# Kernel tuning notes

Hardware: AMD Instinct MI355X
Metric: run time of the kernel (lower is better)

## Reference

```python
import jax, jax.numpy as jnp
import numpy as np

B, N, IN_F, OUT_F, H, NUM_EDGE_TYPES = 16, 512, 256, 256, 8, 50
HEAD_DIM = OUT_F // H
LN_EPS = 1e-5


def setup_inputs() -> dict:
    key = jax.random.key(0)
    ks = jax.random.split(key, 8)
    x = jax.random.normal(ks[0], (B, N, IN_F), dtype=jnp.float32)
    adj = jax.random.randint(ks[1], (B, N, N), 0, 2, dtype=jnp.int32)
    edge_types = jax.random.randint(ks[2], (B, N, N), 0, NUM_EDGE_TYPES, dtype=jnp.int32)
    # Parameters (torch Linear stores weight as [out, in]; we keep [in, out] for x @ W)
    W = jax.random.normal(ks[3], (IN_F, OUT_F), dtype=jnp.float32) / np.sqrt(IN_F)
    a1 = jax.random.normal(ks[4], (HEAD_DIM,), dtype=jnp.float32) / np.sqrt(HEAD_DIM)
    a2 = jax.random.normal(ks[5], (HEAD_DIM,), dtype=jnp.float32) / np.sqrt(HEAD_DIM)
    edge_emb = jax.random.normal(ks[6], (NUM_EDGE_TYPES, H), dtype=jnp.float32) * 0.02
    edge_emb = edge_emb.at[0].set(0.0)  # padding_idx=0
    ln_gamma = jnp.ones((OUT_F,), dtype=jnp.float32)
    ln_beta = jnp.zeros((OUT_F,), dtype=jnp.float32)
    return {"x": x, "adj": adj, "edge_types": edge_types, "W": W, "a1": a1,
            "a2": a2, "edge_emb": edge_emb, "ln_gamma": ln_gamma, "ln_beta": ln_beta}


def reference(x, adj, edge_types, W, a1, a2, edge_emb, ln_gamma, ln_beta):
    Bx, Nx, _ = x.shape
    # Wh: [B, N, H, D]
    Wh = (x @ W).reshape(Bx, Nx, H, HEAD_DIM)
    # per-node attention scalars: [B, N, H]
    s1 = jnp.einsum('bnhd,d->bnh', Wh, a1)
    s2 = jnp.einsum('bnhd,d->bnh', Wh, a2)
    # e: [B, N(i), N(j), H]
    e = s1[:, :, None, :] + s2[:, None, :, :] + edge_emb[edge_types]
    e = jnp.where(e > 0, e, 0.2 * e)  # leaky_relu(0.2)
    e = jnp.where((adj == 0)[..., None], jnp.float32(-1e9), e)
    alpha = jax.nn.softmax(e, axis=2)  # softmax over j
    # (dropout omitted: eval mode / deterministic reference)
    h = jnp.einsum('bijh,bjhd->bihd', alpha, Wh).reshape(Bx, Nx, OUT_F)
    # LayerNorm over last dim
    mu = jnp.mean(h, axis=-1, keepdims=True)
    var = jnp.mean(jnp.square(h - mu), axis=-1, keepdims=True)
    hn = (h - mu) * jax.lax.rsqrt(var + LN_EPS) * ln_gamma + ln_beta
    return jax.nn.elu(hn)
```

## Files before the change

kernel.cpp:

```cpp
#include <hip/hip_runtime.h>
#include <hip/hip_bf16.h>
#include <stdint.h>

namespace gat {
constexpr int NB   = 16;
constexpr int NN   = 512;
constexpr int FIN  = 256;
constexpr int FOUT = 256;
constexpr int H    = 8;
constexpr int NE   = 50;
constexpr float L2E  = 1.4426950408889634f;
constexpr float MASK = -115.41500f;
}
using namespace gat;

typedef __attribute__((ext_vector_type(8))) short short8;
typedef __attribute__((ext_vector_type(4))) float f32x4;

__device__ __forceinline__ unsigned pk_bf16(unsigned ulo, unsigned uhi) {
  return __builtin_amdgcn_perm(uhi, ulo, 0x07060302u);
}
__device__ __forceinline__ unsigned pk2f(float a, float b) {
  return pk_bf16(__float_as_uint(a) + 0x8000u, __float_as_uint(b) + 0x8000u);
}
__device__ __forceinline__ unsigned short bf1(float a) {
  return (unsigned short)((__float_as_uint(a) + 0x8000u) >> 16);
}

__global__ __launch_bounds__(256) void k_pre(const int* __restrict__ adj,
                                             const int* __restrict__ ety,
                                             const float* __restrict__ Wm,
                                             const float* __restrict__ a1,
                                             const float* __restrict__ a2,
                                             unsigned* __restrict__ codes,
                                             unsigned short* __restrict__ WbTa) {
  const int blk = blockIdx.x;
  if (blk < 1024) {
    const size_t base = ((size_t)blk * 256 + threadIdx.x) * 16;
    const int4* ap = (const int4*)(adj + base);
    const int4* ep = (const int4*)(ety + base);
    unsigned o[4];
    #pragma unroll
    for (int g = 0; g < 4; ++g) {
      const int4 a = ap[g];
      const int4 e = ep[g];
      o[g] = (unsigned)(e.x | (a.x << 6))
           | ((unsigned)(e.y | (a.y << 6)) << 8)
           | ((unsigned)(e.z | (a.z << 6)) << 16)
           | ((unsigned)(e.w | (a.w << 6)) << 24);
    }
    uint4 v; v.x = o[0]; v.y = o[1]; v.z = o[2]; v.w = o[3];
    *(uint4*)(codes + base / 4) = v;
  } else if (blk < 1280) {
    const int k = blk - 1024;
    const int f = threadIdx.x;
    WbTa[f * FIN + k] = bf1(Wm[k * FOUT + f]);
  } else {
    const int k = threadIdx.x;
    const float* wr = Wm + (size_t)k * FOUT;
    #pragma unroll
    for (int h = 0; h < H; ++h) {
      float v1 = 0.f, v2 = 0.f;
      #pragma unroll
      for (int d = 0; d < 32; ++d) {
        const float wv = wr[h * 32 + d];
        v1 += wv * a1[d];
        v2 += wv * a2[d];
      }
      WbTa[(256 + h) * FIN + k] = bf1(v1);
      WbTa[(264 + h) * FIN + k] = bf1(v2);
    }
  }
}

__global__ __launch_bounds__(256, 4) void k_gemm(
    const float* __restrict__ x, const unsigned short* __restrict__ WbTa,
    unsigned short* __restrict__ WhT, float* __restrict__ s1T, float* __restrict__ s2T)
{
  __shared__ alignas(16) unsigned short xS[16 * 264];
  const int t    = threadIdx.x;
  const int row0 = blockIdx.x * 16;

  {
    const int r  = t >> 4;
    const int kb = (t & 15) * 16;
    const float4* xg = (const float4*)(x + (size_t)(row0 + r) * FIN + kb);
    const float4 v0 = xg[0], v1 = xg[1], v2 = xg[2], v3 = xg[3];
    uint4 o0, o1;
    o0.x = pk2f(v0.x, v0.y); o0.y = pk2f(v0.z, v0.w);
    o0.z = pk2f(v1.x, v1.y); o0.w = pk2f(v1.z, v1.w);
    o1.x = pk2f(v2.x, v2.y); o1.y = pk2f(v2.z, v2.w);
    o1.z = pk2f(v3.x, v3.y); o1.w = pk2f(v3.z, v3.w);
    *(uint4*)&xS[r * 264 + kb]     = o0;
    *(uint4*)&xS[r * 264 + kb + 8] = o1;
  }
  __syncthreads();

  const int w    = t >> 6;
  const int L    = t & 63;
  const int nn   = L & 15;
  const int quad = L >> 4;
  const unsigned short* wb = WbTa + (size_t)(w * 64 + nn) * FIN + quad * 8;
  const unsigned short* wa = WbTa + (size_t)(256 + nn) * FIN + quad * 8;
  const unsigned short* xp = &xS[nn * 264 + quad * 8];

  f32x4 acc0 = {0.f,0.f,0.f,0.f}, acc1 = {0.f,0.f,0.f,0.f};
  f32x4 acc2 = {0.f,0.f,0.f,0.f}, acc3 = {0.f,0.f,0.f,0.f};
  f32x4 accA = {0.f,0.f,0.f,0.f};

  #pragma unroll
  for (int kc = 0; kc < 8; ++kc) {
    const int k0 = kc * 32;
    const short8 A  = *(const short8*)(xp + k0);
    const short8 B0 = *(const short8*)(wb + k0);
    const short8 B1 = *(const short8*)(wb + 16 * FIN + k0);
    const short8 B2 = *(const short8*)(wb + 32 * FIN + k0);
    const short8 B3 = *(const short8*)(wb + 48 * FIN + k0);
    acc0 = __builtin_amdgcn_mfma_f32_16x16x32_bf16(A, B0, acc0, 0, 0, 0);
    acc1 = __builtin_amdgcn_mfma_f32_16x16x32_bf16(A, B1, acc1, 0, 0, 0);
    acc2 = __builtin_amdgcn_mfma_f32_16x16x32_bf16(A, B2, acc2, 0, 0, 0);
    acc3 = __builtin_amdgcn_mfma_f32_16x16x32_bf16(A, B3, acc3, 0, 0, 0);
    if (w == 3) {
      const short8 BA = *(const short8*)(wa + k0);
      accA = __builtin_amdgcn_mfma_f32_16x16x32_bf16(A, BA, accA, 0, 0, 0);
    }
  }

  const int b     = row0 >> 9;
  const int node0 = (row0 & 511) + quad * 4;
  f32x4 accs[4] = {acc0, acc1, acc2, acc3};

  #pragma unroll
  for (int ft = 0; ft < 4; ++ft) {
    const int f = w * 64 + ft * 16 + nn;
    uint2 o;
    o.x = pk2f(accs[ft][0], accs[ft][1]);
    o.y = pk2f(accs[ft][2], accs[ft][3]);
    *(uint2*)(WhT + (size_t)((b * 8 + (f >> 5)) * 32 + (f & 31)) * 512 + node0) = o;
  }

  if (w == 3) {
    float4 sv;
    sv.x = accA[0] * L2E; sv.y = accA[1] * L2E;
    sv.z = accA[2] * L2E; sv.w = accA[3] * L2E;
    float* dst = (nn < 8) ? (s1T + (size_t)(b * 8 + nn) * 512 + node0)
                          : (s2T + (size_t)(b * 8 + (nn - 8)) * 512 + node0);
    *(float4*)dst = sv;
  }
}

__global__ __launch_bounds__(512, 4) void k_attn(
    const unsigned char* __restrict__ codes,
    const float* __restrict__ s1T, const float* __restrict__ s2T,
    const unsigned short* __restrict__ WhT, const float* __restrict__ emb,
    const float* __restrict__ gam, const float* __restrict__ bet,
    float* __restrict__ out)
{
  __shared__ float2 embS[4 * 64];
  __shared__ float2 lnS[16 * 4];
  __shared__ float  s2S[8 * 512];
  __shared__ float  redS[256 * 18];

  const int t    = threadIdx.x;
  const int b    = blockIdx.x >> 5;
  const int i0   = (blockIdx.x & 31) * 16;
  const int W    = t >> 6;
  const int w    = W & 3;
  const int jh   = W >> 2;
  const int L    = t & 63;
  const int i    = L & 15;
  const int quad = L >> 4;
  const int h0   = w, h1 = w + 4;

  {
    const float4* sg = (const float4*)(s2T + (size_t)b * 8 * 512);
    float4* ss = (float4*)s2S;
    ss[t]       = sg[t];
    ss[t + 512] = sg[t + 512];
  }
  if (t < 256) {
    const int wp = t >> 6, e = t & 63;
    if (e < NE) {
      float2 v; v.x = emb[e * H + wp] * L2E; v.y = emb[e * H + wp + 4] * L2E;
      embS[t] = v;
    }
  }

  const int row   = b * NN + i0 + i;
  const int jbase = jh * 256;

  uint2 cw[8];
  {
    const unsigned char* cp = codes + (size_t)row * NN + jbase + quad * 8;
    #pragma unroll
    for (int kc = 0; kc < 8; ++kc) cw[kc] = *(const uint2*)(cp + kc * 32);
  }

  const float si0 = s1T[(size_t)(b * 8 + h0) * 512 + i0 + i];
  const float si1 = s1T[(size_t)(b * 8 + h1) * 512 + i0 + i];
  const unsigned short* wt00 = WhT + (size_t)((b * 8 + h0) * 32 + i)      * 512;
  const unsigned short* wt01 = WhT + (size_t)((b * 8 + h0) * 32 + 16 + i) * 512;
  const unsigned short* wt10 = WhT + (size_t)((b * 8 + h1) * 32 + i)      * 512;
  const unsigned short* wt11 = WhT + (size_t)((b * 8 + h1) * 32 + 16 + i) * 512;

  f32x4 acc00 = {0.f,0.f,0.f,0.f}, acc01 = {0.f,0.f,0.f,0.f};
  f32x4 acc10 = {0.f,0.f,0.f,0.f}, acc11 = {0.f,0.f,0.f,0.f};
  float l0 = 0.f, l1 = 0.f;

  const int ja0 = jbase + quad * 8;
  short8 nA00 = *(const short8*)(wt00 + ja0);
  short8 nA01 = *(const short8*)(wt01 + ja0);
  short8 nA10 = *(const short8*)(wt10 + ja0);
  short8 nA11 = *(const short8*)(wt11 + ja0);

  __syncthreads();

  #pragma unroll
  for (int kc = 0; kc < 8; ++kc) {
    const int ja  = jbase + kc * 32 + quad * 8;
    const short8 A00 = nA00, A01 = nA01, A10 = nA10, A11 = nA11;
    {
      const int jn = ja + 32;
      nA00 = *(const short8*)(wt00 + jn);
      nA01 = *(const short8*)(wt01 + jn);
      nA10 = *(const short8*)(wt10 + jn);
      nA11 = *(const short8*)(wt11 + jn);
    }
    const float4 sa0 = *(const float4*)&s2S[h0 * 512 + ja];
    const float4 sb0 = *(const float4*)&s2S[h0 * 512 + ja + 4];
    const float4 sa1 = *(const float4*)&s2S[h1 * 512 + ja];
    const float4 sb1 = *(const float4*)&s2S[h1 * 512 + ja + 4];

    const float s20[8] = {sa0.x, sa0.y, sa0.z, sa0.w, sb0.x, sb0.y, sb0.z, sb0.w};
    const float s21[8] = {sa1.x, sa1.y, sa1.z, sa1.w, sb1.x, sb1.y, sb1.z, sb1.w};

    unsigned u0[8], u1[8];
    #pragma unroll
    for (int q = 0; q < 8; ++q) {
      const unsigned cword = (q < 4) ? cw[kc].x : cw[kc].y;
      const unsigned c = (cword >> ((q & 3) * 8)) & 0x7fu;
      const bool on = c >= 64u;
      const float2 em = embS[w * 64 + (c & 63u)];
      float e0 = si0 + s20[q] + em.x;
      float e1 = si1 + s21[q] + em.y;
      e0 = fmaxf(e0, 0.2f * e0);
      e1 = fmaxf(e1, 0.2f * e1);
      e0 = on ? e0 : MASK;
      e1 = on ? e1 : MASK;
      const float p0 = exp2f(e0);
      const float p1 = exp2f(e1);
      l0 += p0; l1 += p1;
      u0[q] = __float_as_uint(p0) + 0x8000u;
      u1[q] = __float_as_uint(p1) + 0x8000u;
    }
    uint4 U0, U1;
    U0.x = pk_bf16(u0[0], u0[1]); U0.y = pk_bf16(u0[2], u0[3]);
    U0.z = pk_bf16(u0[4], u0[5]); U0.w = pk_bf16(u0[6], u0[7]);
    U1.x = pk_bf16(u1[0], u1[1]); U1.y = pk_bf16(u1[2], u1[3]);
    U1.z = pk_bf16(u1[4], u1[5]); U1.w = pk_bf16(u1[6], u1[7]);
    const short8 B0 = __builtin_bit_cast(short8, U0);
    const short8 B1 = __builtin_bit_cast(short8, U1);

    acc00 = __builtin_amdgcn_mfma_f32_16x16x32_bf16(A00, B0, acc00, 0, 0, 0);
    acc01 = __builtin_amdgcn_mfma_f32_16x16x32_bf16(A01, B0, acc01, 0, 0, 0);
    acc10 = __builtin_amdgcn_mfma_f32_16x16x32_bf16(A10, B1, acc10, 0, 0, 0);
    acc11 = __builtin_amdgcn_mfma_f32_16x16x32_bf16(A11, B1, acc11, 0, 0, 0);
  }

  l0 += __shfl_xor(l0, 16); l0 += __shfl_xor(l0, 32);
  l1 += __shfl_xor(l1, 16); l1 += __shfl_xor(l1, 32);

  const int tt = (w << 6) | L;
  if (jh == 1) {
    float* rp = redS + tt * 18;
    rp[0]=acc00[0]; rp[1]=acc00[1]; rp[2]=acc00[2]; rp[3]=acc00[3];
    rp[4]=acc01[0]; rp[5]=acc01[1]; rp[6]=acc01[2]; rp[7]=acc01[3];
    rp[8]=acc10[0]; rp[9]=acc10[1]; rp[10]=acc10[2]; rp[11]=acc10[3];
    rp[12]=acc11[0]; rp[13]=acc11[1]; rp[14]=acc11[2]; rp[15]=acc11[3];
    rp[16]=l0; rp[17]=l1;
  }
  __syncthreads();

  float vals[16]; float mu, rstd;
  if (jh == 0) {
    const float* rp = redS + tt * 18;
    acc00[0]+=rp[0]; acc00[1]+=rp[1]; acc00[2]+=rp[2]; acc00[3]+=rp[3];
    acc01[0]+=rp[4]; acc01[1]+=rp[5]; acc01[2]+=rp[6]; acc01[3]+=rp[7];
    acc10[0]+=rp[8]; acc10[1]+=rp[9]; acc10[2]+=rp[10]; acc10[3]+=rp[11];
    acc11[0]+=rp[12]; acc11[1]+=rp[13]; acc11[2]+=rp[14]; acc11[3]+=rp[15];
    l0 += rp[16]; l1 += rp[17];
    const float inv0 = __builtin_amdgcn_rcpf(l0);
    const float inv1 = __builtin_amdgcn_rcpf(l1);
    #pragma unroll
    for (int r = 0; r < 4; ++r) {
      vals[r]      = acc00[r] * inv0;
      vals[4 + r]  = acc01[r] * inv0;
      vals[8 + r]  = acc10[r] * inv1;
      vals[12 + r] = acc11[r] * inv1;
    }
    float s = 0.f, ss = 0.f;
    #pragma unroll
    for (int k = 0; k < 16; ++k) { s += vals[k]; ss += vals[k] * vals[k]; }
    s += __shfl_xor(s, 16); ss += __shfl_xor(ss, 16);
    s += __shfl_xor(s, 32); ss += __shfl_xor(ss, 32);
    if (quad == 0) { float2 v; v.x = s; v.y = ss; lnS[i * 4 + w] = v; }
  }
  __syncthreads();
  if (jh == 1) return;

  {
    float S = 0.f, SS = 0.f;
    #pragma unroll
    for (int ww = 0; ww < 4; ++ww) { const float2 v = lnS[i * 4 + ww]; S += v.x; SS += v.y; }
    mu = S * (1.0f / 256.0f);
    const float var = SS * (1.0f / 256.0f) - mu * mu;
    rstd = rsqrtf(var + 1e-5f);
  }

  const int fb[4] = { h0 * 32 + quad * 4, h0 * 32 + 16 + quad * 4,
                      h1 * 32 + quad * 4, h1 * 32 + 16 + quad * 4 };
  #pragma unroll
  for (int g = 0; g < 4; ++g) {
    const float4 gv = *(const float4*)(gam + fb[g]);
    const float4 bv = *(const float4*)(bet + fb[g]);
    float4 o;
    o.x = (vals[g*4+0] - mu) * rstd * gv.x + bv.x;
    o.y = (vals[g*4+1] - mu) * rstd * gv.y + bv.y;
    o.z = (vals[g*4+2] - mu) * rstd * gv.z + bv.z;
    o.w = (vals[g*4+3] - mu) * rstd * gv.w + bv.w;
    o.x = o.x > 0.f ? o.x : exp2f(o.x * L2E) - 1.f;
    o.y = o.y > 0.f ? o.y : exp2f(o.y * L2E) - 1.f;
    o.z = o.z > 0.f ? o.z : exp2f(o.z * L2E) - 1.f;
    o.w = o.w > 0.f ? o.w : exp2f(o.w * L2E) - 1.f;
    *(float4*)(out + (size_t)row * FOUT + fb[g]) = o;
  }
}

extern "C" void kernel_launch(void* const* d_in, const int* in_sizes, int n_in,
                              void* d_out, int out_size, void* d_ws, size_t ws_size,
                              hipStream_t stream) {
  (void)in_sizes; (void)n_in; (void)out_size; (void)ws_size;
  const float* x   = (const float*)d_in[0];
  const int*   adj = (const int*)  d_in[1];
  const int*   ety = (const int*)  d_in[2];
  const float* Wm  = (const float*)d_in[3];
  const float* a1  = (const float*)d_in[4];
  const float* a2  = (const float*)d_in[5];
  const float* emb = (const float*)d_in[6];
  const float* gam = (const float*)d_in[7];
  const float* bet = (const float*)d_in[8];
  float* out = (float*)d_out;

  unsigned short* WhT  = (unsigned short*)d_ws;
  unsigned short* WbTa = WhT + (size_t)NB * H * 32 * 512;
  float* s1T  = (float*)(WbTa + (size_t)272 * FIN);
  float* s2T  = s1T + (size_t)NB * H * NN;
  unsigned char* codes = (unsigned char*)(s2T + (size_t)NB * H * NN);

  k_pre<<<dim3(1281), dim3(256), 0, stream>>>(adj, ety, Wm, a1, a2, (unsigned*)codes, WbTa);
  k_gemm<<<dim3(NB * NN / 16), dim3(256), 0, stream>>>(x, WbTa, WhT, s1T, s2T);
  k_attn<<<dim3(NB * (NN / 16)), dim3(512), 0, stream>>>(codes, s1T, s2T, WhT, emb, gam, bet, out);
}
```

Measured before the change: 136.8 us.

## Fuse pre, GEMM and attention kernels into one cooperative kernel with grid syncs

Merges the three kernel launches into a single cooperative kernel of 512 blocks of 512 threads. Two grid-wide barriers separate the packing, projection and attention phases. The GEMM phase is reshaped so eight waves each cover 32 output features. The goal is to remove launch gaps and inter-kernel drain time. In exchange it pays for grid-sync overhead, fixes occupancy for every phase at one shape, and needs all 512 blocks co-resident; the old three-kernel path remains as a fallback if the cooperative launch fails.

Measured after the change: 266.8 us. 1.95x slower.

```diff
diff --git a/kernel.cpp b/kernel.cpp
--- a/kernel.cpp
+++ b/kernel.cpp
@@ -1,6 +1,9 @@
 #include <hip/hip_runtime.h>
 #include <hip/hip_bf16.h>
+#include <hip/hip_cooperative_groups.h>
 #include <stdint.h>
+
+namespace cg = cooperative_groups;
 
 namespace gat {
 constexpr int NB   = 16;
@@ -27,16 +30,28 @@
   return (unsigned short)((__float_as_uint(a) + 0x8000u) >> 16);
 }
 
-__global__ __launch_bounds__(256) void k_pre(const int* __restrict__ adj,
-                                             const int* __restrict__ ety,
-                                             const float* __restrict__ Wm,
-                                             const float* __restrict__ a1,
-                                             const float* __restrict__ a2,
-                                             unsigned* __restrict__ codes,
-                                             unsigned short* __restrict__ WbTa) {
+__global__ __launch_bounds__(512, 4) void k_fused(
+    const int* __restrict__ adj, const int* __restrict__ ety,
+    const float* __restrict__ x, const float* __restrict__ Wm,
+    const float* __restrict__ a1, const float* __restrict__ a2,
+    const float* __restrict__ emb, const float* __restrict__ gam,
+    const float* __restrict__ bet, float* __restrict__ out,
+    unsigned short* __restrict__ WhT, unsigned short* __restrict__ WbTa,
+    float* __restrict__ s1T, float* __restrict__ s2T,
+    unsigned char* __restrict__ codes)
+{
+  __shared__ __align__(16) char smem[37376];
+  float2* embS = (float2*)smem;
+  float2* lnS  = (float2*)(smem + 2048);
+  float*  s2S  = (float*)(smem + 2560);
+  float*  redS = (float*)(smem + 18944);
+  unsigned short* xS = (unsigned short*)smem;
+
   const int blk = blockIdx.x;
-  if (blk < 1024) {
-    const size_t base = ((size_t)blk * 256 + threadIdx.x) * 16;
+  const int t   = threadIdx.x;
+
+  {
+    const size_t base = ((size_t)blk * 512 + t) * 16;
     const int4* ap = (const int4*)(adj + base);
     const int4* ep = (const int4*)(ety + base);
     unsigned o[4];
@@ -50,126 +65,94 @@
            | ((unsigned)(e.w | (a.w << 6)) << 24);
     }
     uint4 v; v.x = o[0]; v.y = o[1]; v.z = o[2]; v.w = o[3];
-    *(uint4*)(codes + base / 4) = v;
-  } else if (blk < 1280) {
-    const int k = blk - 1024;
-    const int f = threadIdx.x;
-    WbTa[f * FIN + k] = bf1(Wm[k * FOUT + f]);
-  } else {
-    const int k = threadIdx.x;
-    const float* wr = Wm + (size_t)k * FOUT;
-    #pragma unroll
-    for (int h = 0; h < H; ++h) {
-      float v1 = 0.f, v2 = 0.f;
+    *(uint4*)(codes + base) = v;
+  }
+  if (blk < 256) {
+    if (t < 256) WbTa[t * FIN + blk] = bf1(Wm[blk * FOUT + t]);
+  } else if (blk == 256) {
+    if (t < 256) {
+      const int k = t;
+      const float* wr = Wm + (size_t)k * FOUT;
       #pragma unroll
-      for (int d = 0; d < 32; ++d) {
-        const float wv = wr[h * 32 + d];
-        v1 += wv * a1[d];
-        v2 += wv * a2[d];
+      for (int h = 0; h < H; ++h) {
+        float v1 = 0.f, v2 = 0.f;
+        #pragma unroll
+        for (int d = 0; d < 32; ++d) {
+          const float wv = wr[h * 32 + d];
+          v1 += wv * a1[d];
+          v2 += wv * a2[d];
+        }
+        WbTa[(256 + h) * FIN + k] = bf1(v1);
+        WbTa[(264 + h) * FIN + k] = bf1(v2);
       }
-      WbTa[(256 + h) * FIN + k] = bf1(v1);
-      WbTa[(264 + h) * FIN + k] = bf1(v2);
-    }
-  }
-}
-
-__global__ __launch_bounds__(256, 4) void k_gemm(
-    const float* __restrict__ x, const unsigned short* __restrict__ WbTa,
-    unsigned short* __restrict__ WhT, float* __restrict__ s1T, float* __restrict__ s2T)
-{
-  __shared__ alignas(16) unsigned short xS[16 * 264];
-  const int t    = threadIdx.x;
-  const int row0 = blockIdx.x * 16;
-
-  {
-    const int r  = t >> 4;
-    const int kb = (t & 15) * 16;
+    }
+  }
+  cg::this_grid().sync();
+
+  const int row0 = blk * 16;
+  {
+    const int r  = t >> 5;
+    const int kb = (t & 31) * 8;
     const float4* xg = (const float4*)(x + (size_t)(row0 + r) * FIN + kb);
-    const float4 v0 = xg[0], v1 = xg[1], v2 = xg[2], v3 = xg[3];
-    uint4 o0, o1;
-    o0.x = pk2f(v0.x, v0.y); o0.y = pk2f(v0.z, v0.w);
-    o0.z = pk2f(v1.x, v1.y); o0.w = pk2f(v1.z, v1.w);
-    o1.x = pk2f(v2.x, v2.y); o1.y = pk2f(v2.z, v2.w);
-    o1.z = pk2f(v3.x, v3.y); o1.w = pk2f(v3.z, v3.w);
-    *(uint4*)&xS[r * 264 + kb]     = o0;
-    *(uint4*)&xS[r * 264 + kb + 8] = o1;
-  }
-  __syncthreads();
-
-  const int w    = t >> 6;
+    const float4 v0 = xg[0], v1 = xg[1];
+    uint4 o;
+    o.x = pk2f(v0.x, v0.y); o.y = pk2f(v0.z, v0.w);
+    o.z = pk2f(v1.x, v1.y); o.w = pk2f(v1.z, v1.w);
+    *(uint4*)&xS[r * 264 + kb] = o;
+  }
+  __syncthreads();
+
+  const int W8   = t >> 6;
   const int L    = t & 63;
   const int nn   = L & 15;
   const int quad = L >> 4;
-  const unsigned short* wb = WbTa + (size_t)(w * 64 + nn) * FIN + quad * 8;
-  const unsigned short* wa = WbTa + (size_t)(256 + nn) * FIN + quad * 8;
-  const unsigned short* xp = &xS[nn * 264 + quad * 8];
-
-  f32x4 acc0 = {0.f,0.f,0.f,0.f}, acc1 = {0.f,0.f,0.f,0.f};
-  f32x4 acc2 = {0.f,0.f,0.f,0.f}, acc3 = {0.f,0.f,0.f,0.f};
-  f32x4 accA = {0.f,0.f,0.f,0.f};
-
-  #pragma unroll
-  for (int kc = 0; kc < 8; ++kc) {
-    const int k0 = kc * 32;
-    const short8 A  = *(const short8*)(xp + k0);
-    const short8 B0 = *(const short8*)(wb + k0);
-    const short8 B1 = *(const short8*)(wb + 16 * FIN + k0);
-    const short8 B2 = *(const short8*)(wb + 32 * FIN + k0);
-    const short8 B3 = *(const short8*)(wb + 48 * FIN + k0);
-    acc0 = __builtin_amdgcn_mfma_f32_16x16x32_bf16(A, B0, acc0, 0, 0, 0);
-    acc1 = __builtin_amdgcn_mfma_f32_16x16x32_bf16(A, B1, acc1, 0, 0, 0);
-    acc2 = __builtin_amdgcn_mfma_f32_16x16x32_bf16(A, B2, acc2, 0, 0, 0);
-    acc3 = __builtin_amdgcn_mfma_f32_16x16x32_bf16(A, B3, acc3, 0, 0, 0);
-    if (w == 3) {
-      const short8 BA = *(const short8*)(wa + k0);
-      accA = __builtin_amdgcn_mfma_f32_16x16x32_bf16(A, BA, accA, 0, 0, 0);
-    }
-  }
-
-  const int b     = row0 >> 9;
-  const int node0 = (row0 & 511) + quad * 4;
-  f32x4 accs[4] = {acc0, acc1, acc2, acc3};
-
-  #pragma unroll
-  for (int ft = 0; ft < 4; ++ft) {
-    const int f = w * 64 + ft * 16 + nn;
-    uint2 o;
-    o.x = pk2f(accs[ft][0], accs[ft][1]);
-    o.y = pk2f(accs[ft][2], accs[ft][3]);
-    *(uint2*)(WhT + (size_t)((b * 8 + (f >> 5)) * 32 + (f & 31)) * 512 + node0) = o;
-  }
-
-  if (w == 3) {
-    float4 sv;
-    sv.x = accA[0] * L2E; sv.y = accA[1] * L2E;
-    sv.z = accA[2] * L2E; sv.w = accA[3] * L2E;
-    float* dst = (nn < 8) ? (s1T + (size_t)(b * 8 + nn) * 512 + node0)
-                          : (s2T + (size_t)(b * 8 + (nn - 8)) * 512 + node0);
-    *(float4*)dst = sv;
-  }
-}
-
-__global__ __launch_bounds__(512, 4) void k_attn(
-    const unsigned char* __restrict__ codes,
-    const float* __restrict__ s1T, const float* __restrict__ s2T,
-    const unsigned short* __restrict__ WhT, const float* __restrict__ emb,
-    const float* __restrict__ gam, const float* __restrict__ bet,
-    float* __restrict__ out)
-{
-  __shared__ float2 embS[4 * 64];
-  __shared__ float2 lnS[16 * 4];
-  __shared__ float  s2S[8 * 512];
-  __shared__ float  redS[256 * 18];
-
-  const int t    = threadIdx.x;
-  const int b    = blockIdx.x >> 5;
-  const int i0   = (blockIdx.x & 31) * 16;
-  const int W    = t >> 6;
-  const int w    = W & 3;
-  const int jh   = W >> 2;
-  const int L    = t & 63;
-  const int i    = L & 15;
-  const int quad = L >> 4;
+  {
+    const unsigned short* wb = WbTa + (size_t)(W8 * 32 + nn) * FIN + quad * 8;
+    const unsigned short* wa = WbTa + (size_t)(256 + nn) * FIN + quad * 8;
+    const unsigned short* xp = &xS[nn * 264 + quad * 8];
+
+    f32x4 acc0 = {0.f,0.f,0.f,0.f}, acc1 = {0.f,0.f,0.f,0.f}, accA = {0.f,0.f,0.f,0.f};
+    #pragma unroll
+    for (int kc = 0; kc < 8; ++kc) {
+      const int k0 = kc * 32;
+      const short8 A  = *(const short8*)(xp + k0);
+      const short8 B0 = *(const short8*)(wb + k0);
+      const short8 B1 = *(const short8*)(wb + 16 * FIN + k0);
+      acc0 = __builtin_amdgcn_mfma_f32_16x16x32_bf16(A, B0, acc0, 0, 0, 0);
+      acc1 = __builtin_amdgcn_mfma_f32_16x16x32_bf16(A, B1, acc1, 0, 0, 0);
+      if (W8 == 7) {
+        const short8 BA = *(const short8*)(wa + k0);
+        accA = __builtin_amdgcn_mfma_f32_16x16x32_bf16(A, BA, accA, 0, 0, 0);
+      }
+    }
+
+    const int b     = row0 >> 9;
+    const int node0 = (row0 & 511) + quad * 4;
+    f32x4 accs[2] = {acc0, acc1};
+    #pragma unroll
+    for (int ft = 0; ft < 2; ++ft) {
+      const int f = W8 * 32 + ft * 16 + nn;
+      uint2 o;
+      o.x = pk2f(accs[ft][0], accs[ft][1]);
+      o.y = pk2f(accs[ft][2], accs[ft][3]);
+      *(uint2*)(WhT + (size_t)((b * 8 + (f >> 5)) * 32 + (f & 31)) * 512 + node0) = o;
+    }
+    if (W8 == 7) {
+      float4 sv;
+      sv.x = accA[0] * L2E; sv.y = accA[1] * L2E;
+      sv.z = accA[2] * L2E; sv.w = accA[3] * L2E;
+      float* dst = (nn < 8) ? (s1T + (size_t)(b * 8 + nn) * 512 + node0)
+                            : (s2T + (size_t)(b * 8 + (nn - 8)) * 512 + node0);
+      *(float4*)dst = sv;
+    }
+  }
+  cg::this_grid().sync();
+
+  const int b    = blk >> 5;
+  const int i0   = (blk & 31) * 16;
+  const int w    = W8 & 3;
+  const int jh   = W8 >> 2;
+  const int i    = nn;
   const int h0   = w, h1 = w + 4;
 
   {
@@ -336,13 +319,312 @@
   }
 }
 
+__global__ __launch_bounds__(256) void k_pre(const int* __restrict__ adj,
+                                             const int* __restrict__ ety,
+                                             const float* __restrict__ Wm,
+                                             const float* __restrict__ a1,
+                                             const float* __restrict__ a2,
+                                             unsigned* __restrict__ codes,
+                                             unsigned short* __restrict__ WbTa) {
+  const int blk = blockIdx.x;
+  if (blk < 1024) {
+    const size_t base = ((size_t)blk * 256 + threadIdx.x) * 16;
+    const int4* ap = (const int4*)(adj + base);
+    const int4* ep = (const int4*)(ety + base);
+    unsigned o[4];
+    #pragma unroll
+    for (int g = 0; g < 4; ++g) {
+      const int4 a = ap[g];
+      const int4 e = ep[g];
+      o[g] = (unsigned)(e.x | (a.x << 6))
+           | ((unsigned)(e.y | (a.y << 6)) << 8)
+           | ((unsigned)(e.z | (a.z << 6)) << 16)
+           | ((unsigned)(e.w | (a.w << 6)) << 24);
+    }
+    uint4 v; v.x = o[0]; v.y = o[1]; v.z = o[2]; v.w = o[3];
+    *(uint4*)(codes + base / 4) = v;
+  } else if (blk < 1280) {
+    const int k = blk - 1024;
+    const int f = threadIdx.x;
+    WbTa[f * FIN + k] = bf1(Wm[k * FOUT + f]);
+  } else {
+    const int k = threadIdx.x;
+    const float* wr = Wm + (size_t)k * FOUT;
+    #pragma unroll
+    for (int h = 0; h < H; ++h) {
+      float v1 = 0.f, v2 = 0.f;
+      #pragma unroll
+      for (int d = 0; d < 32; ++d) {
+        const float wv = wr[h * 32 + d];
+        v1 += wv * a1[d];
+        v2 += wv * a2[d];
+      }
+      WbTa[(256 + h) * FIN + k] = bf1(v1);
+      WbTa[(264 + h) * FIN + k] = bf1(v2);
+    }
+  }
+}
+
+__global__ __launch_bounds__(256, 4) void k_gemm(
+    const float* __restrict__ x, const unsigned short* __restrict__ WbTa,
+    unsigned short* __restrict__ WhT, float* __restrict__ s1T, float* __restrict__ s2T)
+{
+  __shared__ alignas(16) unsigned short xS[16 * 264];
+  const int t    = threadIdx.x;
+  const int row0 = blockIdx.x * 16;
+  {
+    const int r  = t >> 4;
+    const int kb = (t & 15) * 16;
+    const float4* xg = (const float4*)(x + (size_t)(row0 + r) * FIN + kb);
+    const float4 v0 = xg[0], v1 = xg[1], v2 = xg[2], v3 = xg[3];
+    uint4 o0, o1;
+    o0.x = pk2f(v0.x, v0.y); o0.y = pk2f(v0.z, v0.w);
+    o0.z = pk2f(v1.x, v1.y); o0.w = pk2f(v1.z, v1.w);
+    o1.x = pk2f(v2.x, v2.y); o1.y = pk2f(v2.z, v2.w);
+    o1.z = pk2f(v3.x, v3.y); o1.w = pk2f(v3.z, v3.w);
+    *(uint4*)&xS[r * 264 + kb]     = o0;
+    *(uint4*)&xS[r * 264 + kb + 8] = o1;
+  }
+  __syncthreads();
+
+  const int w    = t >> 6;
+  const int L    = t & 63;
+  const int nn   = L & 15;
+  const int quad = L >> 4;
+  const unsigned short* wb = WbTa + (size_t)(w * 64 + nn) * FIN + quad * 8;
+  const unsigned short* wa = WbTa + (size_t)(256 + nn) * FIN + quad * 8;
+  const unsigned short* xp = &xS[nn * 264 + quad * 8];
+
+  f32x4 acc0 = {0.f,0.f,0.f,0.f}, acc1 = {0.f,0.f,0.f,0.f};
+  f32x4 acc2 = {0.f,0.f,0.f,0.f}, acc3 = {0.f,0.f,0.f,0.f};
+  f32x4 accA = {0.f,0.f,0.f,0.f};
+
+  #pragma unroll
+  for (int kc = 0; kc < 8; ++kc) {
+    const int k0 = kc * 32;
+    const short8 A  = *(const short8*)(xp + k0);
+    const short8 B0 = *(const short8*)(wb + k0);
+    const short8 B1 = *(const short8*)(wb + 16 * FIN + k0);
+    const short8 B2 = *(const short8*)(wb + 32 * FIN + k0);
+    const short8 B3 = *(const short8*)(wb + 48 * FIN + k0);
+    acc0 = __builtin_amdgcn_mfma_f32_16x16x32_bf16(A, B0, acc0, 0, 0, 0);
+    acc1 = __builtin_amdgcn_mfma_f32_16x16x32_bf16(A, B1, acc1, 0, 0, 0);
+    acc2 = __builtin_amdgcn_mfma_f32_16x16x32_bf16(A, B2, acc2, 0, 0, 0);
+    acc3 = __builtin_amdgcn_mfma_f32_16x16x32_bf16(A, B3, acc3, 0, 0, 0);
+    if (w == 3) {
+      const short8 BA = *(const short8*)(wa + k0);
+      accA = __builtin_amdgcn_mfma_f32_16x16x32_bf16(A, BA, accA, 0, 0, 0);
+    }
+  }
+
+  const int b     = row0 >> 9;
+  const int node0 = (row0 & 511) + quad * 4;
+  f32x4 accs[4] = {acc0, acc1, acc2, acc3};
+  #pragma unroll
+  for (int ft = 0; ft < 4; ++ft) {
+    const int f = w * 64 + ft * 16 + nn;
+    uint2 o;
+    o.x = pk2f(accs[ft][0], accs[ft][1]);
+    o.y = pk2f(accs[ft][2], accs[ft][3]);
+    *(uint2*)(WhT + (size_t)((b * 8 + (f >> 5)) * 32 + (f & 31)) * 512 + node0) = o;
+  }
+  if (w == 3) {
+    float4 sv;
+    sv.x = accA[0] * L2E; sv.y = accA[1] * L2E;
+    sv.z = accA[2] * L2E; sv.w = accA[3] * L2E;
+    float* dst = (nn < 8) ? (s1T + (size_t)(b * 8 + nn) * 512 + node0)
+                          : (s2T + (size_t)(b * 8 + (nn - 8)) * 512 + node0);
+    *(float4*)dst = sv;
+  }
+}
+
+__global__ __launch_bounds__(512, 4) void k_attn(
+    const unsigned char* __restrict__ codes,
+    const float* __restrict__ s1T, const float* __restrict__ s2T,
+    const unsigned short* __restrict__ WhT, const float* __restrict__ emb,
+    const float* __restrict__ gam, const float* __restrict__ bet,
+    float* __restrict__ out)
+{
+  __shared__ float2 embS[4 * 64];
+  __shared__ float2 lnS[16 * 4];
+  __shared__ float  s2S[8 * 512];
+  __shared__ float  redS[256 * 18];
+
+  const int t    = threadIdx.x;
+  const int b    = blockIdx.x >> 5;
+  const int i0   = (blockIdx.x & 31) * 16;
+  const int W    = t >> 6;
+  const int w    = W & 3;
+  const int jh   = W >> 2;
+  const int L    = t & 63;
+  const int i    = L & 15;
+  const int quad = L >> 4;
+  const int h0   = w, h1 = w + 4;
+
+  {
+    const float4* sg = (const float4*)(s2T + (size_t)b * 8 * 512);
+    float4* ss = (float4*)s2S;
+    ss[t]       = sg[t];
+    ss[t + 512] = sg[t + 512];
+  }
+  if (t < 256) {
+    const int wp = t >> 6, e = t & 63;
+    if (e < NE) {
+      float2 v; v.x = emb[e * H + wp] * L2E; v.y = emb[e * H + wp + 4] * L2E;
+      embS[t] = v;
+    }
+  }
+
+  const int row   = b * NN + i0 + i;
+  const int jbase = jh * 256;
+  uint2 cw[8];
+  {
+    const unsigned char* cp = codes + (size_t)row * NN + jbase + quad * 8;
+    #pragma unroll
+    for (int kc = 0; kc < 8; ++kc) cw[kc] = *(const uint2*)(cp + kc * 32);
+  }
+  const float si0 = s1T[(size_t)(b * 8 + h0) * 512 + i0 + i];
+  const float si1 = s1T[(size_t)(b * 8 + h1) * 512 + i0 + i];
+  const unsigned short* wt00 = WhT + (size_t)((b * 8 + h0) * 32 + i)      * 512;
+  const unsigned short* wt01 = WhT + (size_t)((b * 8 + h0) * 32 + 16 + i) * 512;
+  const unsigned short* wt10 = WhT + (size_t)((b * 8 + h1) * 32 + i)      * 512;
+  const unsigned short* wt11 = WhT + (size_t)((b * 8 + h1) * 32 + 16 + i) * 512;
+
+  f32x4 acc00 = {0.f,0.f,0.f,0.f}, acc01 = {0.f,0.f,0.f,0.f};
+  f32x4 acc10 = {0.f,0.f,0.f,0.f}, acc11 = {0.f,0.f,0.f,0.f};
+  float l0 = 0.f, l1 = 0.f;
+
+  const int ja0 = jbase + quad * 8;
+  short8 nA00 = *(const short8*)(wt00 + ja0);
+  short8 nA01 = *(const short8*)(wt01 + ja0);
+  short8 nA10 = *(const short8*)(wt10 + ja0);
+  short8 nA11 = *(const short8*)(wt11 + ja0);
+
+  __syncthreads();
+
+  #pragma unroll
+  for (int kc = 0; kc < 8; ++kc) {
+    const int ja  = jbase + kc * 32 + quad * 8;
+    const short8 A00 = nA00, A01 = nA01, A10 = nA10, A11 = nA11;
+    {
+      const int jn = ja + 32;
+      nA00 = *(const short8*)(wt00 + jn);
+      nA01 = *(const short8*)(wt01 + jn);
+      nA10 = *(const short8*)(wt10 + jn);
+      nA11 = *(const short8*)(wt11 + jn);
+    }
+    const float4 sa0 = *(const float4*)&s2S[h0 * 512 + ja];
+    const float4 sb0 = *(const float4*)&s2S[h0 * 512 + ja + 4];
+    const float4 sa1 = *(const float4*)&s2S[h1 * 512 + ja];
+    const float4 sb1 = *(const float4*)&s2S[h1 * 512 + ja + 4];
+    const float s20[8] = {sa0.x, sa0.y, sa0.z, sa0.w, sb0.x, sb0.y, sb0.z, sb0.w};
+    const float s21[8] = {sa1.x, sa1.y, sa1.z, sa1.w, sb1.x, sb1.y, sb1.z, sb1.w};
+    unsigned u0[8], u1[8];
+    #pragma unroll
+    for (int q = 0; q < 8; ++q) {
+      const unsigned cword = (q < 4) ? cw[kc].x : cw[kc].y;
+      const unsigned c = (cword >> ((q & 3) * 8)) & 0x7fu;
+      const bool on = c >= 64u;
+      const float2 em = embS[w * 64 + (c & 63u)];
+      float e0 = si0 + s20[q] + em.x;
+      float e1 = si1 + s21[q] + em.y;
+      e0 = fmaxf(e0, 0.2f * e0);
+      e1 = fmaxf(e1, 0.2f * e1);
+      e0 = on ? e0 : MASK;
+      e1 = on ? e1 : MASK;
+      const float p0 = exp2f(e0);
+      const float p1 = exp2f(e1);
+      l0 += p0; l1 += p1;
+      u0[q] = __float_as_uint(p0) + 0x8000u;
+      u1[q] = __float_as_uint(p1) + 0x8000u;
+    }
+    uint4 U0, U1;
+    U0.x = pk_bf16(u0[0], u0[1]); U0.y = pk_bf16(u0[2], u0[3]);
+    U0.z = pk_bf16(u0[4], u0[5]); U0.w = pk_bf16(u0[6], u0[7]);
+    U1.x = pk_bf16(u1[0], u1[1]); U1.y = pk_bf16(u1[2], u1[3]);
+    U1.z = pk_bf16(u1[4], u1[5]); U1.w = pk_bf16(u1[6], u1[7]);
+    const short8 B0 = __builtin_bit_cast(short8, U0);
+    const short8 B1 = __builtin_bit_cast(short8, U1);
+    acc00 = __builtin_amdgcn_mfma_f32_16x16x32_bf16(A00, B0, acc00, 0, 0, 0);
+    acc01 = __builtin_amdgcn_mfma_f32_16x16x32_bf16(A01, B0, acc01, 0, 0, 0);
+    acc10 = __builtin_amdgcn_mfma_f32_16x16x32_bf16(A10, B1, acc10, 0, 0, 0);
+    acc11 = __builtin_amdgcn_mfma_f32_16x16x32_bf16(A11, B1, acc11, 0, 0, 0);
+  }
+
+  l0 += __shfl_xor(l0, 16); l0 += __shfl_xor(l0, 32);
+  l1 += __shfl_xor(l1, 16); l1 += __shfl_xor(l1, 32);
+
+  const int tt = (w << 6) | L;
+  if (jh == 1) {
+    float* rp = redS + tt * 18;
+    rp[0]=acc00[0]; rp[1]=acc00[1]; rp[2]=acc00[2]; rp[3]=acc00[3];
+    rp[4]=acc01[0]; rp[5]=acc01[1]; rp[6]=acc01[2]; rp[7]=acc01[3];
+    rp[8]=acc10[0]; rp[9]=acc10[1]; rp[10]=acc10[2]; rp[11]=acc10[3];
+    rp[12]=acc11[0]; rp[13]=acc11[1]; rp[14]=acc11[2]; rp[15]=acc11[3];
+    rp[16]=l0; rp[17]=l1;
+  }
+  __syncthreads();
+
+  float vals[16]; float mu, rstd;
+  if (jh == 0) {
+    const float* rp = redS + tt * 18;
+    acc00[0]+=rp[0]; acc00[1]+=rp[1]; acc00[2]+=rp[2]; acc00[3]+=rp[3];
+    acc01[0]+=rp[4]; acc01[1]+=rp[5]; acc01[2]+=rp[6]; acc01[3]+=rp[7];
+    acc10[0]+=rp[8]; acc10[1]+=rp[9]; acc10[2]+=rp[10]; acc10[3]+=rp[11];
+    acc11[0]+=rp[12]; acc11[1]+=rp[13]; acc11[2]+=rp[14]; acc11[3]+=rp[15];
+    l0 += rp[16]; l1 += rp[17];
+    const float inv0 = __builtin_amdgcn_rcpf(l0);
+    const float inv1 = __builtin_amdgcn_rcpf(l1);
+    #pragma unroll
+    for (int r = 0; r < 4; ++r) {
+      vals[r]      = acc00[r] * inv0;
+      vals[4 + r]  = acc01[r] * inv0;
+      vals[8 + r]  = acc10[r] * inv1;
+      vals[12 + r] = acc11[r] * inv1;
+    }
+    float s = 0.f, ss = 0.f;
+    #pragma unroll
+    for (int k = 0; k < 16; ++k) { s += vals[k]; ss += vals[k] * vals[k]; }
+    s += __shfl_xor(s, 16); ss += __shfl_xor(ss, 16);
+    s += __shfl_xor(s, 32); ss += __shfl_xor(ss, 32);
+    if (quad == 0) { float2 v; v.x = s; v.y = ss; lnS[i * 4 + w] = v; }
+  }
+  __syncthreads();
+  if (jh == 1) return;
+  {
+    float S = 0.f, SS = 0.f;
+    #pragma unroll
+    for (int ww = 0; ww < 4; ++ww) { const float2 v = lnS[i * 4 + ww]; S += v.x; SS += v.y; }
+    mu = S * (1.0f / 256.0f);
+    const float var = SS * (1.0f / 256.0f) - mu * mu;
+    rstd = rsqrtf(var + 1e-5f);
+  }
+  const int fb[4] = { h0 * 32 + quad * 4, h0 * 32 + 16 + quad * 4,
+                      h1 * 32 + quad * 4, h1 * 32 + 16 + quad * 4 };
+  #pragma unroll
+  for (int g = 0; g < 4; ++g) {
+    const float4 gv = *(const float4*)(gam + fb[g]);
+    const float4 bv = *(const float4*)(bet + fb[g]);
+    float4 o;
+    o.x = (vals[g*4+0] - mu) * rstd * gv.x + bv.x;
+    o.y = (vals[g*4+1] - mu) * rstd * gv.y + bv.y;
+    o.z = (vals[g*4+2] - mu) * rstd * gv.z + bv.z;
+    o.w = (vals[g*4+3] - mu) * rstd * gv.w + bv.w;
+    o.x = o.x > 0.f ? o.x : exp2f(o.x * L2E) - 1.f;
+    o.y = o.y > 0.f ? o.y : exp2f(o.y * L2E) - 1.f;
+    o.z = o.z > 0.f ? o.z : exp2f(o.z * L2E) - 1.f;
+    o.w = o.w > 0.f ? o.w : exp2f(o.w * L2E) - 1.f;
+    *(float4*)(out + (size_t)row * FOUT + fb[g]) = o;
+  }
+}
+
 extern "C" void kernel_launch(void* const* d_in, const int* in_sizes, int n_in,
                               void* d_out, int out_size, void* d_ws, size_t ws_size,
                               hipStream_t stream) {
   (void)in_sizes; (void)n_in; (void)out_size; (void)ws_size;
-  const float* x   = (const float*)d_in[0];
   const int*   adj = (const int*)  d_in[1];
   const int*   ety = (const int*)  d_in[2];
+  const float* x   = (const float*)d_in[0];
   const float* Wm  = (const float*)d_in[3];
   const float* a1  = (const float*)d_in[4];
   const float* a2  = (const float*)d_in[5];
@@ -357,7 +639,14 @@
   float* s2T  = s1T + (size_t)NB * H * NN;
   unsigned char* codes = (unsigned char*)(s2T + (size_t)NB * H * NN);
 
-  k_pre<<<dim3(1281), dim3(256), 0, stream>>>(adj, ety, Wm, a1, a2, (unsigned*)codes, WbTa);
-  k_gemm<<<dim3(NB * NN / 16), dim3(256), 0, stream>>>(x, WbTa, WhT, s1T, s2T);
-  k_attn<<<dim3(NB * (NN / 16)), dim3(512), 0, stream>>>(codes, s1T, s2T, WhT, emb, gam, bet, out);
-}
+  void* args[] = { (void*)&adj, (void*)&ety, (void*)&x, (void*)&Wm, (void*)&a1,
+                   (void*)&a2, (void*)&emb, (void*)&gam, (void*)&bet, (void*)&out,
+                   (void*)&WhT, (void*)&WbTa, (void*)&s1T, (void*)&s2T, (void*)&codes };
+  hipError_t err = hipLaunchCooperativeKernel((const void*)k_fused, dim3(512), dim3(512),
+                                              args, 0, stream);
+  if (err != hipSuccess) {
+    k_pre<<<dim3(1281), dim3(256), 0, stream>>>(adj, ety, Wm, a1, a2, (unsigned*)codes, WbTa);
+    k_gemm<<<dim3(NB * NN / 16), dim3(256), 0, stream>>>(x, WbTa, WhT, s1T, s2T);
+    k_attn<<<dim3(NB * (NN / 16)), dim3(512), 0, stream>>>(codes, s1T, s2T, WhT, emb, gam, bet, out);
+  }
+}
```

## Fold mask into embedding table, compute softmax denominators via MFMA, merge pre-pass into GEMM

Applied to the files above, without the earlier changes.

Moves the adj/edge-type packing from the weight pre-pass into the GEMM launch as extra blocks, so the large packing work can run alongside the GEMM blocks in one launch. In the attention loop, the adjacency mask is folded into a 128-entry per-head embedding table, where masked entries hold a large negative bias, and this removes the per-element select. The row sums of exp are now taken by an extra MFMA against a ones vector, on the same bf16-truncated probabilities used for the weighted sum, which replaces the scalar accumulation and shuffles. Rounding is replaced by truncation plus a small bias added to the table entries, which changes numerics slightly.

Measured after the change: 138.4 us. About the same (+1.2%).

```diff
diff --git a/kernel.cpp b/kernel.cpp
--- a/kernel.cpp
+++ b/kernel.cpp
@@ -10,7 +10,8 @@
 constexpr int H    = 8;
 constexpr int NE   = 50;
 constexpr float L2E  = 1.4426950408889634f;
-constexpr float MASK = -115.41500f;
+constexpr float MASKB = -192.0f;
+constexpr float RBIAS = 0.00281502f;
 }
 using namespace gat;
 
@@ -27,32 +28,13 @@
   return (unsigned short)((__float_as_uint(a) + 0x8000u) >> 16);
 }
 
-__global__ __launch_bounds__(256) void k_pre(const int* __restrict__ adj,
-                                             const int* __restrict__ ety,
-                                             const float* __restrict__ Wm,
-                                             const float* __restrict__ a1,
-                                             const float* __restrict__ a2,
-                                             unsigned* __restrict__ codes,
-                                             unsigned short* __restrict__ WbTa) {
+__global__ __launch_bounds__(256) void k_prew(const float* __restrict__ Wm,
+                                              const float* __restrict__ a1,
+                                              const float* __restrict__ a2,
+                                              unsigned short* __restrict__ WbTa) {
   const int blk = blockIdx.x;
-  if (blk < 1024) {
-    const size_t base = ((size_t)blk * 256 + threadIdx.x) * 16;
-    const int4* ap = (const int4*)(adj + base);
-    const int4* ep = (const int4*)(ety + base);
-    unsigned o[4];
-    #pragma unroll
-    for (int g = 0; g < 4; ++g) {
-      const int4 a = ap[g];
-      const int4 e = ep[g];
-      o[g] = (unsigned)(e.x | (a.x << 6))
-           | ((unsigned)(e.y | (a.y << 6)) << 8)
-           | ((unsigned)(e.z | (a.z << 6)) << 16)
-           | ((unsigned)(e.w | (a.w << 6)) << 24);
-    }
-    uint4 v; v.x = o[0]; v.y = o[1]; v.z = o[2]; v.w = o[3];
-    *(uint4*)(codes + base / 4) = v;
-  } else if (blk < 1280) {
-    const int k = blk - 1024;
+  if (blk < 256) {
+    const int k = blk;
     const int f = threadIdx.x;
     WbTa[f * FIN + k] = bf1(Wm[k * FOUT + f]);
   } else {
@@ -73,14 +55,34 @@
   }
 }
 
-__global__ __launch_bounds__(256, 4) void k_gemm(
+__global__ __launch_bounds__(256, 4) void k_gp(
     const float* __restrict__ x, const unsigned short* __restrict__ WbTa,
-    unsigned short* __restrict__ WhT, float* __restrict__ s1T, float* __restrict__ s2T)
+    const int* __restrict__ adj, const int* __restrict__ ety,
+    unsigned short* __restrict__ WhT, float* __restrict__ s1T, float* __restrict__ s2T,
+    unsigned* __restrict__ codes)
 {
+  const int t = threadIdx.x;
+  if (blockIdx.x >= 512) {
+    const size_t base = ((size_t)(blockIdx.x - 512) * 256 + t) * 16;
+    const int4* ap = (const int4*)(adj + base);
+    const int4* ep = (const int4*)(ety + base);
+    unsigned o[4];
+    #pragma unroll
+    for (int g = 0; g < 4; ++g) {
+      const int4 a = ap[g];
+      const int4 e = ep[g];
+      o[g] = (unsigned)(e.x | (a.x << 6))
+           | ((unsigned)(e.y | (a.y << 6)) << 8)
+           | ((unsigned)(e.z | (a.z << 6)) << 16)
+           | ((unsigned)(e.w | (a.w << 6)) << 24);
+    }
+    uint4 v; v.x = o[0]; v.y = o[1]; v.z = o[2]; v.w = o[3];
+    *(uint4*)(codes + base / 4) = v;
+    return;
+  }
+
   __shared__ alignas(16) unsigned short xS[16 * 264];
-  const int t    = threadIdx.x;
   const int row0 = blockIdx.x * 16;
-
   {
     const int r  = t >> 4;
     const int kb = (t & 15) * 16;
@@ -129,7 +131,6 @@
   const int b     = row0 >> 9;
   const int node0 = (row0 & 511) + quad * 4;
   f32x4 accs[4] = {acc0, acc1, acc2, acc3};
-
   #pragma unroll
   for (int ft = 0; ft < 4; ++ft) {
     const int f = w * 64 + ft * 16 + nn;
@@ -138,7 +139,6 @@
     o.y = pk2f(accs[ft][2], accs[ft][3]);
     *(uint2*)(WhT + (size_t)((b * 8 + (f >> 5)) * 32 + (f & 31)) * 512 + node0) = o;
   }
-
   if (w == 3) {
     float4 sv;
     sv.x = accA[0] * L2E; sv.y = accA[1] * L2E;
@@ -156,7 +156,7 @@
     const float* __restrict__ gam, const float* __restrict__ bet,
     float* __restrict__ out)
 {
-  __shared__ float2 embS[4 * 64];
+  __shared__ float2 embS[4 * 128];
   __shared__ float2 lnS[16 * 4];
   __shared__ float  s2S[8 * 512];
   __shared__ float  redS[256 * 18];
@@ -178,24 +178,26 @@
     ss[t]       = sg[t];
     ss[t + 512] = sg[t + 512];
   }
-  if (t < 256) {
-    const int wp = t >> 6, e = t & 63;
-    if (e < NE) {
-      float2 v; v.x = emb[e * H + wp] * L2E; v.y = emb[e * H + wp + 4] * L2E;
-      embS[t] = v;
-    }
+  {
+    const int wp = t >> 7, c = t & 127;
+    float2 v;
+    if (c >= 64 && c < 64 + NE) {
+      v.x = emb[(c - 64) * H + wp]     * L2E + RBIAS;
+      v.y = emb[(c - 64) * H + wp + 4] * L2E + RBIAS;
+    } else {
+      v.x = MASKB; v.y = MASKB;
+    }
+    embS[t] = v;
   }
 
   const int row   = b * NN + i0 + i;
   const int jbase = jh * 256;
-
   uint2 cw[8];
   {
     const unsigned char* cp = codes + (size_t)row * NN + jbase + quad * 8;
     #pragma unroll
     for (int kc = 0; kc < 8; ++kc) cw[kc] = *(const uint2*)(cp + kc * 32);
   }
-
   const float si0 = s1T[(size_t)(b * 8 + h0) * 512 + i0 + i];
   const float si1 = s1T[(size_t)(b * 8 + h1) * 512 + i0 + i];
   const unsigned short* wt00 = WhT + (size_t)((b * 8 + h0) * 32 + i)      * 512;
@@ -205,7 +207,9 @@
 
   f32x4 acc00 = {0.f,0.f,0.f,0.f}, acc01 = {0.f,0.f,0.f,0.f};
   f32x4 acc10 = {0.f,0.f,0.f,0.f}, acc11 = {0.f,0.f,0.f,0.f};
-  float l0 = 0.f, l1 = 0.f;
+  f32x4 accL0 = {0.f,0.f,0.f,0.f}, accL1 = {0.f,0.f,0.f,0.f};
+  const short one_bf = (short)0x3F80;
+  const short8 ONES = {one_bf, one_bf, one_bf, one_bf, one_bf, one_bf, one_bf, one_bf};
 
   const int ja0 = jbase + quad * 8;
   short8 nA00 = *(const short8*)(wt00 + ja0);
@@ -230,7 +234,6 @@
     const float4 sb0 = *(const float4*)&s2S[h0 * 512 + ja + 4];
     const float4 sa1 = *(const float4*)&s2S[h1 * 512 + ja];
     const float4 sb1 = *(const float4*)&s2S[h1 * 512 + ja + 4];
-
     const float s20[8] = {sa0.x, sa0.y, sa0.z, sa0.w, sb0.x, sb0.y, sb0.z, sb0.w};
     const float s21[8] = {sa1.x, sa1.y, sa1.z, sa1.w, sb1.x, sb1.y, sb1.z, sb1.w};
 
@@ -238,20 +241,14 @@
     #pragma unroll
     for (int q = 0; q < 8; ++q) {
       const unsigned cword = (q < 4) ? cw[kc].x : cw[kc].y;
-      const unsigned c = (cword >> ((q & 3) * 8)) & 0x7fu;
-      const bool on = c >= 64u;
-      const float2 em = embS[w * 64 + (c & 63u)];
+      const unsigned c = (cword >> ((q & 3) * 8)) & 0xffu;
+      const float2 em = embS[w * 128 + c];
       float e0 = si0 + s20[q] + em.x;
       float e1 = si1 + s21[q] + em.y;
       e0 = fmaxf(e0, 0.2f * e0);
       e1 = fmaxf(e1, 0.2f * e1);
-      e0 = on ? e0 : MASK;
-      e1 = on ? e1 : MASK;
-      const float p0 = exp2f(e0);
-      const float p1 = exp2f(e1);
-      l0 += p0; l1 += p1;
-      u0[q] = __float_as_uint(p0) + 0x8000u;
-      u1[q] = __float_as_uint(p1) + 0x8000u;
+      u0[q] = __float_as_uint(exp2f(e0));
+      u1[q] = __float_as_uint(exp2f(e1));
     }
     uint4 U0, U1;
     U0.x = pk_bf16(u0[0], u0[1]); U0.y = pk_bf16(u0[2], u0[3]);
@@ -265,10 +262,12 @@
     acc01 = __builtin_amdgcn_mfma_f32_16x16x32_bf16(A01, B0, acc01, 0, 0, 0);
     acc10 = __builtin_amdgcn_mfma_f32_16x16x32_bf16(A10, B1, acc10, 0, 0, 0);
     acc11 = __builtin_amdgcn_mfma_f32_16x16x32_bf16(A11, B1, acc11, 0, 0, 0);
-  }
-
-  l0 += __shfl_xor(l0, 16); l0 += __shfl_xor(l0, 32);
-  l1 += __shfl_xor(l1, 16); l1 += __shfl_xor(l1, 32);
+    accL0 = __builtin_amdgcn_mfma_f32_16x16x32_bf16(ONES, B0, accL0, 0, 0, 0);
+    accL1 = __builtin_amdgcn_mfma_f32_16x16x32_bf16(ONES, B1, accL1, 0, 0, 0);
+  }
+
+  const float l0 = accL0[0];
+  const float l1 = accL1[0];
 
   const int tt = (w << 6) | L;
   if (jh == 1) {
@@ -288,9 +287,8 @@
     acc01[0]+=rp[4]; acc01[1]+=rp[5]; acc01[2]+=rp[6]; acc01[3]+=rp[7];
     acc10[0]+=rp[8]; acc10[1]+=rp[9]; acc10[2]+=rp[10]; acc10[3]+=rp[11];
     acc11[0]+=rp[12]; acc11[1]+=rp[13]; acc11[2]+=rp[14]; acc11[3]+=rp[15];
-    l0 += rp[16]; l1 += rp[17];
-    const float inv0 = __builtin_amdgcn_rcpf(l0);
-    const float inv1 = __builtin_amdgcn_rcpf(l1);
+    const float inv0 = __builtin_amdgcn_rcpf(l0 + rp[16]);
+    const float inv1 = __builtin_amdgcn_rcpf(l1 + rp[17]);
     #pragma unroll
     for (int r = 0; r < 4; ++r) {
       vals[r]      = acc00[r] * inv0;
@@ -307,7 +305,6 @@
   }
   __syncthreads();
   if (jh == 1) return;
-
   {
     float S = 0.f, SS = 0.f;
     #pragma unroll
@@ -316,7 +313,6 @@
     const float var = SS * (1.0f / 256.0f) - mu * mu;
     rstd = rsqrtf(var + 1e-5f);
   }
-
   const int fb[4] = { h0 * 32 + quad * 4, h0 * 32 + 16 + quad * 4,
                       h1 * 32 + quad * 4, h1 * 32 + 16 + quad * 4 };
   #pragma unroll
@@ -357,7 +353,7 @@
   float* s2T  = s1T + (size_t)NB * H * NN;
   unsigned char* codes = (unsigned char*)(s2T + (size_t)NB * H * NN);
 
-  k_pre<<<dim3(1281), dim3(256), 0, stream>>>(adj, ety, Wm, a1, a2, (unsigned*)codes, WbTa);
-  k_gemm<<<dim3(NB * NN / 16), dim3(256), 0, stream>>>(x, WbTa, WhT, s1T, s2T);
+  k_prew<<<dim3(257),  dim3(256), 0, stream>>>(Wm, a1, a2, WbTa);
+  k_gp  <<<dim3(1536), dim3(256), 0, stream>>>(x, WbTa, adj, ety, WhT, s1T, s2T, (unsigned*)codes);
   k_attn<<<dim3(NB * (NN / 16)), dim3(512), 0, stream>>>(codes, s1T, s2T, WhT, emb, gam, bet, out);
 }
```
